# Optimization experiments

Measured on AMD Instinct MI355X. Metric: run time of the kernel, lower is better.

## Reference

```python
import jax, jax.numpy as jnp
import numpy as np

NUM_NODES = 512
HEADS = 4
IN_F = 256
OUT_F = 128
EPS = 1e-5


def _layernorm(x, g, b):
    mu = jnp.mean(x, axis=-1, keepdims=True)
    var = jnp.mean(jnp.square(x - mu), axis=-1, keepdims=True)
    return (x - mu) * jax.lax.rsqrt(var + EPS) * g + b


def setup_inputs() -> dict:
    key = jax.random.key(0)
    ks = jax.random.split(key, 16)
    N = 32 * NUM_NODES
    E = 262144
    s = 0.05
    return {
        "x": jax.random.normal(ks[0], (N, IN_F), jnp.float32),
        "edge_index": jax.random.randint(ks[1], (2, E), 0, N, jnp.int64),
        "W_l": jax.random.normal(ks[2], (IN_F, HEADS * OUT_F), jnp.float32) * s,
        "W_r": jax.random.normal(ks[3], (IN_F, HEADS * OUT_F), jnp.float32) * s,
        "att": jax.random.normal(ks[4], (HEADS, OUT_F), jnp.float32) * s,
        "gat_bias": jnp.zeros((OUT_F,), jnp.float32),
        "gat_gamma": jnp.ones((OUT_F,), jnp.float32),
        "gat_beta": jnp.zeros((OUT_F,), jnp.float32),
        "cnn_W": jax.random.normal(ks[5], (IN_F, OUT_F), jnp.float32) * s,
        "cnn_b": jnp.zeros((OUT_F,), jnp.float32),
        "conv_W": jax.random.normal(ks[6], (OUT_F, OUT_F, 7), jnp.float32) * s,
        "conv_b": jnp.zeros((OUT_F,), jnp.float32),
        "cnn_gamma": jnp.ones((OUT_F,), jnp.float32),
        "cnn_beta": jnp.zeros((OUT_F,), jnp.float32),
        "res_W": jax.random.normal(ks[7], (IN_F, OUT_F), jnp.float32) * s,
        "res_b": jnp.zeros((OUT_F,), jnp.float32),
        "fuse_gamma": jnp.ones((OUT_F,), jnp.float32),
        "fuse_beta": jnp.zeros((OUT_F,), jnp.float32),
    }


def reference(x, edge_index, W_l, W_r, att, gat_bias, gat_gamma, gat_beta,
              cnn_W, cnn_b, conv_W, conv_b, cnn_gamma, cnn_beta,
              res_W, res_b, fuse_gamma, fuse_beta):
    N = x.shape[0]
    B = N // NUM_NODES
    # --- GATv2 branch (add self-loops like PyG default) ---
    loop = jnp.arange(N, dtype=edge_index.dtype)
    src = jnp.concatenate([edge_index[0], loop])
    dst = jnp.concatenate([edge_index[1], loop])
    x_l = (x @ W_l).reshape(N, HEADS, OUT_F)
    x_r = (x @ W_r).reshape(N, HEADS, OUT_F)
    e = x_l[src] + x_r[dst]                      # [E+N, H, F]
    e = jnp.where(e > 0, e, 0.2 * e)             # leaky_relu, slope 0.2
    score = jnp.einsum('ehf,hf->eh', e, att)     # [E+N, H]
    m = jax.ops.segment_max(score, dst, num_segments=N)
    ex = jnp.exp(score - m[dst])
    denom = jax.ops.segment_sum(ex, dst, num_segments=N)
    alpha = ex / denom[dst]
    agg = jax.ops.segment_sum(alpha[:, :, None] * x_l[src], dst, num_segments=N)
    h_gat = jnp.mean(agg, axis=1) + gat_bias     # concat=False -> head mean
    h_gat = jnp.where(h_gat > 0, h_gat, 0.01 * h_gat)  # nn.LeakyReLU default
    h_gat = _layernorm(h_gat, gat_gamma, gat_beta)
    # --- CNN branch ---
    xc = x @ cnn_W + cnn_b                       # [N, F]
    xc = xc.reshape(B, NUM_NODES, OUT_F).transpose(0, 2, 1)  # [B, F, L]
    hc = jax.lax.conv_general_dilated(xc, conv_W, window_strides=(1,),
                                      padding=[(3, 3)],
                                      dimension_numbers=('NCW', 'OIW', 'NCW'))
    hc = hc + conv_b[None, :, None]
    hc = hc.transpose(0, 2, 1).reshape(N, OUT_F)
    hc = jax.nn.relu(hc)
    hc = _layernorm(hc, cnn_gamma, cnn_beta)
    # --- fuse + residual ---
    h = h_gat + hc + (x @ res_W + res_b)
    return _layernorm(h, fuse_gamma, fuse_beta)
```

## Files before the change

### kernel.cpp

```cpp
#include <hip/hip_runtime.h>
#include <hip/hip_bf16.h>
#include <math.h>

#define IN_F 256
#define OUT_F 128
#define HEADS 4
#define HF 512
#define NCAT 1280

typedef __hip_bfloat16 bf16;
typedef unsigned short ushort_t;
typedef unsigned char uchar_t;

using bf16x8 = __attribute__((ext_vector_type(8))) short;
using f32x4  = __attribute__((ext_vector_type(4))) float;

__device__ __forceinline__ float bflo(unsigned u) { return __uint_as_float(u << 16); }
__device__ __forceinline__ float bfhi(unsigned u) { return __uint_as_float(u & 0xffff0000u); }
__device__ __forceinline__ float bf2f(ushort_t u) { return __uint_as_float((unsigned)u << 16); }
__device__ __forceinline__ ushort_t f2bf(float f) {
    __hip_bfloat16 h = __float2bfloat16(f);
    return *reinterpret_cast<ushort_t*>(&h);
}

__device__ __forceinline__ void gload16(const void* g, void* l) {
    __builtin_amdgcn_global_load_lds(
        (const __attribute__((address_space(1))) unsigned int*)g,
        (__attribute__((address_space(3))) unsigned int*)l, 16, 0, 0);
}

template <int CTRL>
__device__ __forceinline__ float dpp_add(float s) {
    int t = __builtin_amdgcn_update_dpp(0, __float_as_int(s), CTRL, 0xf, 0xf, true);
    return s + __int_as_float(t);
}
__device__ __forceinline__ float rowsum16(float s) {
    s = dpp_add<0x121>(s);
    s = dpp_add<0x122>(s);
    s = dpp_add<0x124>(s);
    s = dpp_add<0x128>(s);
    return s;
}

__global__ __launch_bounds__(256) void prep_kernel(
    const float* __restrict__ x, ushort_t* __restrict__ xb, int n_cvt,
    const float* __restrict__ Wl, const float* __restrict__ Wr,
    const float* __restrict__ Wc, const float* __restrict__ Wres,
    const float* __restrict__ Wconv,
    ushort_t* __restrict__ Wt, ushort_t* __restrict__ Wt2,
    const int* __restrict__ ei, int* __restrict__ counts, int E,
    int g1, int g2) {
    int b = blockIdx.x;
    if (b < g1) {
        int i = (b * 256 + threadIdx.x) * 8;
        if (i >= n_cvt) return;
        float4 a = *(const float4*)(x + i);
        float4 c = *(const float4*)(x + i + 4);
        uint4 o;
        o.x = f2bf(a.x) | ((unsigned)f2bf(a.y) << 16);
        o.y = f2bf(a.z) | ((unsigned)f2bf(a.w) << 16);
        o.z = f2bf(c.x) | ((unsigned)f2bf(c.y) << 16);
        o.w = f2bf(c.z) | ((unsigned)f2bf(c.w) << 16);
        *(uint4*)(xb + i) = o;
    } else if (b < g2) {
        int idx = (b - g1) * 256 + threadIdx.x;
        if (idx < NCAT * 256) {
            int n = idx >> 8, k = idx & 255;
            float v;
            if (n < 512)       v = Wl[(size_t)k * 512 + n];
            else if (n < 1024) v = Wr[(size_t)k * 512 + (n - 512)];
            else if (n < 1152) v = Wc[(size_t)k * 128 + (n - 1024)];
            else               v = Wres[(size_t)k * 128 + (n - 1152)];
            Wt[idx] = f2bf(v);
        } else {
            int j = idx - NCAT * 256;
            if (j < 7 * 128 * 128) {
                int k = j >> 14, o = (j >> 7) & 127, i = j & 127;
                Wt2[j] = f2bf(Wconv[((size_t)o * 128 + i) * 7 + k]);
            }
        }
    } else {
        int e = (b - g2) * 256 + threadIdx.x;
        if (e < E) atomicAdd(&counts[ei[E + e]], 1);
    }
}

__global__ __launch_bounds__(256) void mfma_gemm(
    const ushort_t* __restrict__ A,
    const ushort_t* __restrict__ Wt,
    uchar_t* __restrict__ xl8t, float* __restrict__ scales,
    ushort_t* __restrict__ xrb, ushort_t* __restrict__ xcb,
    ushort_t* __restrict__ resb, int M) {
    __shared__ __align__(1024) ushort_t As[128 * 64];
    __shared__ __align__(1024) ushort_t Bs[128 * 64];
    __shared__ float smax[128][2];
    int tid = threadIdx.x;
    int lane = tid & 63, wid = tid >> 6;
    int wr = (wid >> 1) * 64, wc = (wid & 1) * 64;
    int brow = blockIdx.y * 128, bcol = blockIdx.x * 128;
    int srow = lane >> 3;
    int sslot = lane & 7;
    int rl = lane & 15, kq = lane >> 4;
    f32x4 acc[4][4] = {};
    for (int k0 = 0; k0 < 256; k0 += 64) {
        #pragma unroll
        for (int j = 0; j < 4; ++j) {
            int r = (wid * 4 + j) * 8 + srow;
            int sl = sslot ^ (r & 7);
            gload16(A  + (size_t)(brow + r) * 256 + k0 + sl * 8,
                    (char*)As + (wid * 4 + j) * 1024);
            gload16(Wt + (size_t)(bcol + r) * 256 + k0 + sl * 8,
                    (char*)Bs + (wid * 4 + j) * 1024);
        }
        __syncthreads();
        #pragma unroll
        for (int ks = 0; ks < 2; ++ks) {
            int cb = ks * 64 + kq * 16;
            bf16x8 af[4], bfv[4];
            #pragma unroll
            for (int m = 0; m < 4; ++m) {
                int r = wr + m * 16 + rl;
                af[m] = *(const bf16x8*)((const char*)As + r * 128 + (cb ^ ((r & 7) << 4)));
            }
            #pragma unroll
            for (int n = 0; n < 4; ++n) {
                int r = wc + n * 16 + rl;
                bfv[n] = *(const bf16x8*)((const char*)Bs + r * 128 + (cb ^ ((r & 7) << 4)));
            }
            #pragma unroll
            for (int m = 0; m < 4; ++m)
                #pragma unroll
                for (int n = 0; n < 4; ++n)
                    acc[m][n] = __builtin_amdgcn_mfma_f32_16x16x32_bf16(
                        af[m], bfv[n], acc[m][n], 0, 0, 0);
        }
        __syncthreads();
    }
    int rowb = kq * 4;
    if (bcol < 512) {
        int head = bcol >> 7;
        float rmax[4][4];
        #pragma unroll
        for (int m = 0; m < 4; ++m)
            #pragma unroll
            for (int q = 0; q < 4; ++q) {
                float t = fabsf(acc[m][0][q]);
                t = fmaxf(t, fabsf(acc[m][1][q]));
                t = fmaxf(t, fabsf(acc[m][2][q]));
                t = fmaxf(t, fabsf(acc[m][3][q]));
                #pragma unroll
                for (int o = 1; o < 16; o <<= 1) t = fmaxf(t, __shfl_xor(t, o));
                rmax[m][q] = t;
            }
        if (rl == 0) {
            #pragma unroll
            for (int m = 0; m < 4; ++m)
                #pragma unroll
                for (int q = 0; q < 4; ++q)
                    smax[wr + m * 16 + rowb + q][wid & 1] = rmax[m][q];
        }
        __syncthreads();
        #pragma unroll
        for (int m = 0; m < 4; ++m)
            #pragma unroll
            for (int q = 0; q < 4; ++q) {
                int row = wr + m * 16 + rowb + q;
                float sm = fmaxf(fmaxf(smax[row][0], smax[row][1]), 1e-8f);
                float s = sm * (1.f / 127.f);
                float rs = 127.f / sm;
                if ((wid & 1) == 0 && rl == 0)
                    scales[(size_t)(brow + row) * 4 + head] = s;
                #pragma unroll
                for (int n = 0; n < 4; ++n) {
                    int col = bcol + wc + n * 16 + rl;
                    int qv = (int)rintf(acc[m][n][q] * rs) + 128;
                    xl8t[(size_t)(brow + row) * 512 + col] = (uchar_t)qv;
                }
            }
        return;
    }
    ushort_t* dstp; int cstride, cb2;
    if (bcol < 1024)      { dstp = xrb;  cstride = 512; cb2 = bcol - 512; }
    else if (bcol < 1152) { dstp = xcb;  cstride = 128; cb2 = bcol - 1024; }
    else                  { dstp = resb; cstride = 128; cb2 = bcol - 1152; }
    #pragma unroll
    for (int m = 0; m < 4; ++m)
        #pragma unroll
        for (int n = 0; n < 4; ++n) {
            int col = cb2 + wc + n * 16 + rl;
            #pragma unroll
            for (int q = 0; q < 4; ++q) {
                int row = brow + wr + m * 16 + rowb + q;
                dstp[(size_t)row * cstride + col] = f2bf(acc[m][n][q]);
            }
        }
}

__global__ __launch_bounds__(1024) void scan_kernel(
    const int* __restrict__ counts, int* __restrict__ offs,
    int* __restrict__ cursor, int N) {
    __shared__ int wsum[16];
    int t = threadIdx.x;
    int lane = t & 63, w = t >> 6;
    int base = t * 16;
    int local[16], s = 0;
    #pragma unroll
    for (int i = 0; i < 16; ++i) {
        int v = (base + i < N) ? counts[base + i] : 0;
        local[i] = v; s += v;
    }
    int sc = s;
    #pragma unroll
    for (int off = 1; off < 64; off <<= 1) {
        int v = __shfl_up(sc, off);
        if (lane >= off) sc += v;
    }
    if (lane == 63) wsum[w] = sc;
    __syncthreads();
    if (w == 0 && lane < 16) {
        int v = wsum[lane];
        int scv = v;
        #pragma unroll
        for (int off = 1; off < 16; off <<= 1) {
            int u = __shfl_up(scv, off);
            if (lane >= off) scv += u;
        }
        wsum[lane] = scv - v;
    }
    __syncthreads();
    int run = wsum[w] + sc - s;
    #pragma unroll
    for (int i = 0; i < 16; ++i) {
        if (base + i < N) { offs[base + i] = run; cursor[base + i] = run; }
        run += local[i];
    }
}

__global__ __launch_bounds__(256) void scatter_kernel(
    const int* __restrict__ ei, int* __restrict__ cursor,
    int* __restrict__ srcs, int E) {
    int e = blockIdx.x * 256 + threadIdx.x;
    if (e < E) {
        int d = ei[E + e];
        int p = atomicAdd(&cursor[d], 1);
        srcs[p] = ei[e];
    }
}

__global__ __launch_bounds__(256) void conv_ln_kernel(
    const ushort_t* __restrict__ xcb, const float* __restrict__ cnn_b,
    const ushort_t* __restrict__ Wt2, const float* __restrict__ conv_b,
    const float* __restrict__ cnn_gamma, const float* __restrict__ cnn_beta,
    ushort_t* __restrict__ hcn_ln) {
    __shared__ ushort_t As[38][136];
    __shared__ __align__(1024) ushort_t Bs[128 * 128];
    __shared__ float hbuf[32][129];
    int tid = threadIdx.x;
    int lane = tid & 63, wid = tid >> 6;
    int wr = (wid >> 1) * 16, wc = (wid & 1) * 64;
    int b = blockIdx.y, l0 = blockIdx.x * 32;
    for (int u = tid; u < 38 * 16; u += 256) {
        int r = u >> 4, seg = u & 15;
        int l = l0 - 3 + r;
        uint4 o4 = make_uint4(0, 0, 0, 0);
        if (l >= 0 && l < 512) {
            uint4 v = *(const uint4*)(xcb + (size_t)(b * 512 + l) * 128 + seg * 8);
            float4 b0 = *(const float4*)(cnn_b + seg * 8);
            float4 b1 = *(const float4*)(cnn_b + seg * 8 + 4);
            o4.x = f2bf(bflo(v.x) + b0.x) | ((unsigned)f2bf(bfhi(v.x) + b0.y) << 16);
            o4.y = f2bf(bflo(v.y) + b0.z) | ((unsigned)f2bf(bfhi(v.y) + b0.w) << 16);
            o4.z = f2bf(bflo(v.z) + b1.x) | ((unsigned)f2bf(bfhi(v.z) + b1.y) << 16);
            o4.w = f2bf(bflo(v.w) + b1.z) | ((unsigned)f2bf(bfhi(v.w) + b1.w) << 16);
        }
        *(uint4*)&As[r][seg * 8] = o4;
    }
    f32x4 acc[4] = {};
    int rl = lane & 15, kb = (lane >> 4) * 8;
    int sr4 = lane >> 4, ss = lane & 15;
    for (int k = 0; k < 7; ++k) {
        __syncthreads();
        #pragma unroll
        for (int j = 0; j < 8; ++j) {
            int r = (wid * 8 + j) * 4 + sr4;
            int sl = ss ^ (r & 15);
            gload16(Wt2 + ((size_t)(k * 128 + r)) * 128 + sl * 8,
                    (char*)Bs + (wid * 8 + j) * 1024);
        }
        __syncthreads();
        #pragma unroll
        for (int kk = 0; kk < 4; ++kk) {
            bf16x8 af = *(const bf16x8*)&As[wr + rl + k][kk * 32 + kb];
            int cbyte = kk * 64 + (lane >> 4) * 16;
            #pragma unroll
            for (int n = 0; n < 4; ++n) {
                int r = wc + n * 16 + rl;
                bf16x8 bfr = *(const bf16x8*)((const char*)Bs + r * 256
                                              + (cbyte ^ ((r & 15) << 4)));
                acc[n] = __builtin_amdgcn_mfma_f32_16x16x32_bf16(af, bfr, acc[n], 0, 0, 0);
            }
        }
    }
    __syncthreads();
    int rowb = (lane >> 4) * 4;
    #pragma unroll
    for (int n = 0; n < 4; ++n) {
        int col = wc + n * 16 + rl;
        float cb = conv_b[col];
        #pragma unroll
        for (int q = 0; q < 4; ++q) {
            int r = wr + rowb + q;
            hbuf[r][col] = fmaxf(acc[n][q] + cb, 0.f);
        }
    }
    __syncthreads();
    for (int r = wid * 8; r < wid * 8 + 8; ++r) {
        int grow = b * 512 + l0 + r;
        float h0 = hbuf[r][lane], h1 = hbuf[r][lane + 64];
        float s = h0 + h1;
        #pragma unroll
        for (int off = 32; off; off >>= 1) s += __shfl_xor(s, off);
        float mu = s * (1.f / 128.f);
        float d0 = h0 - mu, d1 = h1 - mu;
        float vs = d0 * d0 + d1 * d1;
        #pragma unroll
        for (int off = 32; off; off >>= 1) vs += __shfl_xor(vs, off);
        float inv = rsqrtf(vs * (1.f / 128.f) + 1e-5f);
        size_t base = (size_t)grow * 128;
        hcn_ln[base + lane]      = f2bf(d0 * inv * cnn_gamma[lane]      + cnn_beta[lane]);
        hcn_ln[base + lane + 64] = f2bf(d1 * inv * cnn_gamma[lane + 64] + cnn_beta[lane + 64]);
    }
}

__global__ __launch_bounds__(256) void gat_final_kernel(
    const uchar_t* __restrict__ xl8t, const float* __restrict__ scales,
    const ushort_t* __restrict__ xrb,
    const int* __restrict__ srcs, const int* __restrict__ offs,
    const float* __restrict__ att, const float* __restrict__ gat_bias,
    const float* __restrict__ gat_gamma, const float* __restrict__ gat_beta,
    const ushort_t* __restrict__ hcn_ln, const ushort_t* __restrict__ resb,
    const float* __restrict__ res_b,
    const float* __restrict__ fuse_gamma, const float* __restrict__ fuse_beta,
    float* __restrict__ out, int E, int N) {
    int wid = (blockIdx.x * 256 + threadIdx.x) >> 6;
    int lane = threadIdx.x & 63;
    if (wid >= N) return;
    int d = wid;
    int h = lane >> 4;
    const uint4 rv = ((const uint4*)(xrb + (size_t)d * HF))[lane];
    float xr8[8];
    xr8[0] = bflo(rv.x); xr8[1] = bfhi(rv.x);
    xr8[2] = bflo(rv.y); xr8[3] = bfhi(rv.y);
    xr8[4] = bflo(rv.z); xr8[5] = bfhi(rv.z);
    xr8[6] = bflo(rv.w); xr8[7] = bfhi(rv.w);
    const float LOG2E = 1.44269504f;
    const float4 a0 = ((const float4*)att)[lane * 2];
    const float4 a1 = ((const float4*)att)[lane * 2 + 1];
    const float aw[8] = {a0.x * LOG2E, a0.y * LOG2E, a0.z * LOG2E, a0.w * LOG2E,
                         a1.x * LOG2E, a1.y * LOG2E, a1.z * LOG2E, a1.w * LOG2E};
    float acc[8] = {};
    float dn = 0.f, sumexs = 0.f;

    auto process = [&](uint2 lv, float sc) {
        float qf[8];
        qf[0] = (float)(lv.x & 0xff);         qf[1] = (float)((lv.x >> 8) & 0xff);
        qf[2] = (float)((lv.x >> 16) & 0xff); qf[3] = (float)(lv.x >> 24);
        qf[4] = (float)(lv.y & 0xff);         qf[5] = (float)((lv.y >> 8) & 0xff);
        qf[6] = (float)((lv.y >> 16) & 0xff); qf[7] = (float)(lv.y >> 24);
        float c = 128.f * sc;
        float s1 = 0.f, s2 = 0.f;
        #pragma unroll
        for (int j = 0; j < 8; ++j) {
            float v = fmaf(sc, qf[j], xr8[j]) - c;
            s1 = fmaf(v, aw[j], s1);
            s2 = fmaf(fabsf(v), aw[j], s2);
        }
        float s = fmaf(0.6f, s1, 0.4f * s2);
        s = rowsum16(s);
        float ex = exp2f(s);
        float exs = ex * sc;
        dn += ex; sumexs += exs;
        #pragma unroll
        for (int j = 0; j < 8; ++j) acc[j] = fmaf(exs, qf[j], acc[j]);
    };

    process(((const uint2*)(xl8t + (size_t)d * 512))[lane],
            scales[(size_t)d * 4 + h]);

    int start = offs[d];
    int end = (d == N - 1) ? E : offs[d + 1];
    int p = start;
    for (; p + 3 < end; p += 4) {
        int s0 = srcs[p], s1 = srcs[p + 1], s2 = srcs[p + 2], s3 = srcs[p + 3];
        uint2 l0 = ((const uint2*)(xl8t + (size_t)s0 * 512))[lane];
        uint2 l1 = ((const uint2*)(xl8t + (size_t)s1 * 512))[lane];
        uint2 l2 = ((const uint2*)(xl8t + (size_t)s2 * 512))[lane];
        uint2 l3 = ((const uint2*)(xl8t + (size_t)s3 * 512))[lane];
        float c0 = scales[(size_t)s0 * 4 + h];
        float c1 = scales[(size_t)s1 * 4 + h];
        float c2 = scales[(size_t)s2 * 4 + h];
        float c3 = scales[(size_t)s3 * 4 + h];
        process(l0, c0); process(l1, c1); process(l2, c2); process(l3, c3);
    }
    for (; p < end; ++p) {
        int sp = srcs[p];
        process(((const uint2*)(xl8t + (size_t)sp * 512))[lane],
                scales[(size_t)sp * 4 + h]);
    }

    float inv = 1.f / dn;
    float corr = 128.f * sumexs;
    float v[8];
    #pragma unroll
    for (int j = 0; j < 8; ++j) {
        float t2 = (acc[j] - corr) * inv;
        t2 += __shfl_xor(t2, 16);
        t2 += __shfl_xor(t2, 32);
        v[j] = t2;
    }
    int col = (lane & 15) * 8 + 2 * h;
    float g0 = 0.25f * v[2 * h]     + gat_bias[col];
    float g1 = 0.25f * v[2 * h + 1] + gat_bias[col + 1];
    g0 = g0 > 0.f ? g0 : 0.01f * g0;
    g1 = g1 > 0.f ? g1 : 0.01f * g1;
    float s = g0 + g1;
    #pragma unroll
    for (int off = 32; off; off >>= 1) s += __shfl_xor(s, off);
    float mu = s * (1.f / 128.f);
    float d0 = g0 - mu, d1 = g1 - mu;
    float vs = d0 * d0 + d1 * d1;
    #pragma unroll
    for (int off = 32; off; off >>= 1) vs += __shfl_xor(vs, off);
    float rinv = rsqrtf(vs * (1.f / 128.f) + 1e-5f);
    float hg0 = d0 * rinv * gat_gamma[col]     + gat_beta[col];
    float hg1 = d1 * rinv * gat_gamma[col + 1] + gat_beta[col + 1];
    size_t base = (size_t)d * 128 + col;
    unsigned hcu = *(const unsigned*)(hcn_ln + base);
    unsigned rsu = *(const unsigned*)(resb + base);
    float v0 = hg0 + bflo(hcu) + bflo(rsu) + res_b[col];
    float v1 = hg1 + bfhi(hcu) + bfhi(rsu) + res_b[col + 1];
    s = v0 + v1;
    #pragma unroll
    for (int off = 32; off; off >>= 1) s += __shfl_xor(s, off);
    mu = s * (1.f / 128.f);
    d0 = v0 - mu; d1 = v1 - mu;
    vs = d0 * d0 + d1 * d1;
    #pragma unroll
    for (int off = 32; off; off >>= 1) vs += __shfl_xor(vs, off);
    rinv = rsqrtf(vs * (1.f / 128.f) + 1e-5f);
    float2 o2 = make_float2(d0 * rinv * fuse_gamma[col]     + fuse_beta[col],
                            d1 * rinv * fuse_gamma[col + 1] + fuse_beta[col + 1]);
    *(float2*)(out + base) = o2;
}

extern "C" void kernel_launch(void* const* d_in, const int* in_sizes, int n_in,
                              void* d_out, int out_size, void* d_ws, size_t ws_size,
                              hipStream_t stream) {
    const float* x         = (const float*)d_in[0];
    const int*   ei        = (const int*)d_in[1];
    const float* W_l       = (const float*)d_in[2];
    const float* W_r       = (const float*)d_in[3];
    const float* att       = (const float*)d_in[4];
    const float* gat_bias  = (const float*)d_in[5];
    const float* gat_gamma = (const float*)d_in[6];
    const float* gat_beta  = (const float*)d_in[7];
    const float* cnn_W     = (const float*)d_in[8];
    const float* cnn_b     = (const float*)d_in[9];
    const float* conv_W    = (const float*)d_in[10];
    const float* conv_b    = (const float*)d_in[11];
    const float* cnn_gamma = (const float*)d_in[12];
    const float* cnn_beta  = (const float*)d_in[13];
    const float* res_W     = (const float*)d_in[14];
    const float* res_b     = (const float*)d_in[15];
    const float* fuse_gamma= (const float*)d_in[16];
    const float* fuse_beta = (const float*)d_in[17];

    int N = in_sizes[0] / IN_F;
    int E = in_sizes[1] / 2;

    char* ws = (char*)d_ws;
    size_t off = 0;
    ushort_t* xb     = (ushort_t*)(ws + off); off += (size_t)N * IN_F * 2;
    ushort_t* Wt     = (ushort_t*)(ws + off); off += (size_t)NCAT * IN_F * 2;
    ushort_t* Wt2    = (ushort_t*)(ws + off); off += (size_t)7 * 128 * 128 * 2;
    uchar_t*  xl8t   = (uchar_t*)(ws + off);  off += (size_t)N * HF;
    float*    scales = (float*)(ws + off);    off += (size_t)N * 4 * 4;
    ushort_t* xrb    = (ushort_t*)(ws + off); off += (size_t)N * HF * 2;
    ushort_t* xcb    = (ushort_t*)(ws + off); off += (size_t)N * 128 * 2;
    ushort_t* resb   = (ushort_t*)(ws + off); off += (size_t)N * 128 * 2;
    ushort_t* hcn_ln = (ushort_t*)(ws + off); off += (size_t)N * 128 * 2;
    int*  counts     = (int*)(ws + off);  off += (size_t)N * 4;
    int*  offs       = (int*)(ws + off);  off += (size_t)N * 4;
    int*  cursor     = (int*)(ws + off);  off += (size_t)N * 4;
    int*  srcs       = (int*)(ws + off);  off += (size_t)E * 4;

    hipMemsetAsync(counts, 0, (size_t)N * 4, stream);

    dim3 blk(256);
    int n_cvt = N * IN_F;
    int g1 = (n_cvt / 8 + 255) / 256;
    int g2 = g1 + (NCAT * 256 + 7 * 128 * 128 + 255) / 256;
    int g3 = g2 + (E + 255) / 256;
    prep_kernel<<<g3, blk, 0, stream>>>(x, xb, n_cvt,
        W_l, W_r, cnn_W, res_W, conv_W, Wt, Wt2, ei, counts, E, g1, g2);

    scan_kernel<<<1, 1024, 0, stream>>>(counts, offs, cursor, N);
    scatter_kernel<<<(E + 255) / 256, blk, 0, stream>>>(ei, cursor, srcs, E);

    mfma_gemm<<<dim3(NCAT / 128, N / 128), blk, 0, stream>>>(
        xb, Wt, xl8t, scales, xrb, xcb, resb, N);

    conv_ln_kernel<<<dim3(16, 32), blk, 0, stream>>>(
        xcb, cnn_b, Wt2, conv_b, cnn_gamma, cnn_beta, hcn_ln);

    gat_final_kernel<<<(N + 3) / 4, blk, 0, stream>>>(
        xl8t, scales, xrb, srcs, offs, att, gat_bias, gat_gamma, gat_beta,
        hcn_ln, resb, res_b, fuse_gamma, fuse_beta, (float*)d_out, E, N);
}
```

Before: 142.3 us.

## Split each node's edge list across two waves and combine via shared memory

```diff
diff --git a/kernel.cpp b/kernel.cpp
--- a/kernel.cpp
+++ b/kernel.cpp
@@ -341,10 +341,11 @@
     const float* __restrict__ res_b,
     const float* __restrict__ fuse_gamma, const float* __restrict__ fuse_beta,
     float* __restrict__ out, int E, int N) {
-    int wid = (blockIdx.x * 256 + threadIdx.x) >> 6;
-    int lane = threadIdx.x & 63;
-    if (wid >= N) return;
-    int d = wid;
+    __shared__ float comb[2][10][64];
+    int tid = threadIdx.x;
+    int lane = tid & 63, wid = tid >> 6;
+    int pair = wid >> 1, half = wid & 1;
+    int d = blockIdx.x * 2 + pair;
     int h = lane >> 4;
     const uint4 rv = ((const uint4*)(xrb + (size_t)d * HF))[lane];
     float xr8[8];
@@ -383,13 +384,17 @@
         for (int j = 0; j < 8; ++j) acc[j] = fmaf(exs, qf[j], acc[j]);
     };
 
-    process(((const uint2*)(xl8t + (size_t)d * 512))[lane],
-            scales[(size_t)d * 4 + h]);
+    if (half == 0)
+        process(((const uint2*)(xl8t + (size_t)d * 512))[lane],
+                scales[(size_t)d * 4 + h]);
 
     int start = offs[d];
     int end = (d == N - 1) ? E : offs[d + 1];
-    int p = start;
-    for (; p + 3 < end; p += 4) {
+    int mid = start + ((end - start) >> 1);
+    int ps = half ? mid : start;
+    int pe = half ? end : mid;
+    int p = ps;
+    for (; p + 3 < pe; p += 4) {
         int s0 = srcs[p], s1 = srcs[p + 1], s2 = srcs[p + 2], s3 = srcs[p + 3];
         uint2 l0 = ((const uint2*)(xl8t + (size_t)s0 * 512))[lane];
         uint2 l1 = ((const uint2*)(xl8t + (size_t)s1 * 512))[lane];
@@ -401,11 +406,24 @@
         float c3 = scales[(size_t)s3 * 4 + h];
         process(l0, c0); process(l1, c1); process(l2, c2); process(l3, c3);
     }
-    for (; p < end; ++p) {
+    for (; p < pe; ++p) {
         int sp = srcs[p];
         process(((const uint2*)(xl8t + (size_t)sp * 512))[lane],
                 scales[(size_t)sp * 4 + h]);
     }
+
+    if (half == 1) {
+        #pragma unroll
+        for (int j = 0; j < 8; ++j) comb[pair][j][lane] = acc[j];
+        comb[pair][8][lane] = dn;
+        comb[pair][9][lane] = sumexs;
+    }
+    __syncthreads();
+    if (half == 1) return;
+    #pragma unroll
+    for (int j = 0; j < 8; ++j) acc[j] += comb[pair][j][lane];
+    dn += comb[pair][8][lane];
+    sumexs += comb[pair][9][lane];
 
     float inv = 1.f / dn;
     float corr = 128.f * sumexs;
@@ -512,7 +530,7 @@
     conv_ln_kernel<<<dim3(16, 32), blk, 0, stream>>>(
         xcb, cnn_b, Wt2, conv_b, cnn_gamma, cnn_beta, hcn_ln);
 
-    gat_final_kernel<<<(N + 3) / 4, blk, 0, stream>>>(
+    gat_final_kernel<<<N / 2, blk, 0, stream>>>(
         xl8t, scales, xrb, srcs, offs, att, gat_bias, gat_gamma, gat_beta,
         hcn_ln, resb, res_b, fuse_gamma, fuse_beta, (float*)d_out, E, N);
 }
```

Result: slower. 153.5 us (+7.9%).

## Merge edge scatter into GEMM launch and software-pipeline GAT neighbor loads

Applied to the files above, without the earlier changes.

```diff
diff --git a/kernel.cpp b/kernel.cpp
--- a/kernel.cpp
+++ b/kernel.cpp
@@ -85,19 +85,32 @@
     }
 }
 
-__global__ __launch_bounds__(256) void mfma_gemm(
+__global__ __launch_bounds__(256) void gemm_scatter_kernel(
     const ushort_t* __restrict__ A,
     const ushort_t* __restrict__ Wt,
     uchar_t* __restrict__ xl8t, float* __restrict__ scales,
     ushort_t* __restrict__ xrb, ushort_t* __restrict__ xcb,
-    ushort_t* __restrict__ resb, int M) {
+    ushort_t* __restrict__ resb,
+    const int* __restrict__ ei, int* __restrict__ cursor,
+    int* __restrict__ srcs, int E, int SB) {
     __shared__ __align__(1024) ushort_t As[128 * 64];
     __shared__ __align__(1024) ushort_t Bs[128 * 64];
     __shared__ float smax[128][2];
+    if (blockIdx.x < SB) {
+        int e = blockIdx.x * 256 + threadIdx.x;
+        if (e < E) {
+            int dd = ei[E + e];
+            int pp = atomicAdd(&cursor[dd], 1);
+            srcs[pp] = ei[e];
+        }
+        return;
+    }
+    int bid = blockIdx.x - SB;
+    int by = bid / 10, bx = bid - by * 10;
     int tid = threadIdx.x;
     int lane = tid & 63, wid = tid >> 6;
     int wr = (wid >> 1) * 64, wc = (wid & 1) * 64;
-    int brow = blockIdx.y * 128, bcol = blockIdx.x * 128;
+    int brow = by * 128, bcol = bx * 128;
     int srow = lane >> 3;
     int sslot = lane & 7;
     int rl = lane & 15, kq = lane >> 4;
@@ -233,17 +246,6 @@
     for (int i = 0; i < 16; ++i) {
         if (base + i < N) { offs[base + i] = run; cursor[base + i] = run; }
         run += local[i];
-    }
-}
-
-__global__ __launch_bounds__(256) void scatter_kernel(
-    const int* __restrict__ ei, int* __restrict__ cursor,
-    int* __restrict__ srcs, int E) {
-    int e = blockIdx.x * 256 + threadIdx.x;
-    if (e < E) {
-        int d = ei[E + e];
-        int p = atomicAdd(&cursor[d], 1);
-        srcs[p] = ei[e];
     }
 }
 
@@ -388,18 +390,39 @@
 
     int start = offs[d];
     int end = (d == N - 1) ? E : offs[d + 1];
+    int nfull = (end - start) >> 2;
     int p = start;
-    for (; p + 3 < end; p += 4) {
+    uint2 L0, L1, L2, L3;
+    float C0, C1, C2, C3;
+    if (nfull > 0) {
         int s0 = srcs[p], s1 = srcs[p + 1], s2 = srcs[p + 2], s3 = srcs[p + 3];
-        uint2 l0 = ((const uint2*)(xl8t + (size_t)s0 * 512))[lane];
-        uint2 l1 = ((const uint2*)(xl8t + (size_t)s1 * 512))[lane];
-        uint2 l2 = ((const uint2*)(xl8t + (size_t)s2 * 512))[lane];
-        uint2 l3 = ((const uint2*)(xl8t + (size_t)s3 * 512))[lane];
-        float c0 = scales[(size_t)s0 * 4 + h];
-        float c1 = scales[(size_t)s1 * 4 + h];
-        float c2 = scales[(size_t)s2 * 4 + h];
-        float c3 = scales[(size_t)s3 * 4 + h];
-        process(l0, c0); process(l1, c1); process(l2, c2); process(l3, c3);
+        L0 = ((const uint2*)(xl8t + (size_t)s0 * 512))[lane];
+        L1 = ((const uint2*)(xl8t + (size_t)s1 * 512))[lane];
+        L2 = ((const uint2*)(xl8t + (size_t)s2 * 512))[lane];
+        L3 = ((const uint2*)(xl8t + (size_t)s3 * 512))[lane];
+        C0 = scales[(size_t)s0 * 4 + h];
+        C1 = scales[(size_t)s1 * 4 + h];
+        C2 = scales[(size_t)s2 * 4 + h];
+        C3 = scales[(size_t)s3 * 4 + h];
+        p += 4;
+    }
+    for (int b = 1; b < nfull; ++b) {
+        int s0 = srcs[p], s1 = srcs[p + 1], s2 = srcs[p + 2], s3 = srcs[p + 3];
+        uint2 M0 = ((const uint2*)(xl8t + (size_t)s0 * 512))[lane];
+        uint2 M1 = ((const uint2*)(xl8t + (size_t)s1 * 512))[lane];
+        uint2 M2 = ((const uint2*)(xl8t + (size_t)s2 * 512))[lane];
+        uint2 M3 = ((const uint2*)(xl8t + (size_t)s3 * 512))[lane];
+        float D0 = scales[(size_t)s0 * 4 + h];
+        float D1 = scales[(size_t)s1 * 4 + h];
+        float D2 = scales[(size_t)s2 * 4 + h];
+        float D3 = scales[(size_t)s3 * 4 + h];
+        p += 4;
+        process(L0, C0); process(L1, C1); process(L2, C2); process(L3, C3);
+        L0 = M0; L1 = M1; L2 = M2; L3 = M3;
+        C0 = D0; C1 = D1; C2 = D2; C3 = D3;
+    }
+    if (nfull > 0) {
+        process(L0, C0); process(L1, C1); process(L2, C2); process(L3, C3);
     }
     for (; p < end; ++p) {
         int sp = srcs[p];
@@ -504,10 +527,10 @@
         W_l, W_r, cnn_W, res_W, conv_W, Wt, Wt2, ei, counts, E, g1, g2);
 
     scan_kernel<<<1, 1024, 0, stream>>>(counts, offs, cursor, N);
-    scatter_kernel<<<(E + 255) / 256, blk, 0, stream>>>(ei, cursor, srcs, E);
-
-    mfma_gemm<<<dim3(NCAT / 128, N / 128), blk, 0, stream>>>(
-        xb, Wt, xl8t, scales, xrb, xcb, resb, N);
+
+    int SB = (E + 255) / 256;
+    gemm_scatter_kernel<<<SB + (NCAT / 128) * (N / 128), blk, 0, stream>>>(
+        xb, Wt, xl8t, scales, xrb, xcb, resb, ei, cursor, srcs, E, SB);
 
     conv_ln_kernel<<<dim3(16, 32), blk, 0, stream>>>(
         xcb, cnn_b, Wt2, conv_b, cnn_gamma, cnn_beta, hcn_ln);
```

After: 139.5 us. -2.0%, faster.

## Merge independent kernels into heterogeneous launches and split out final fuse layernorm

Applied to the files above, without the earlier changes.

```diff
diff --git a/kernel.cpp b/kernel.cpp
--- a/kernel.cpp
+++ b/kernel.cpp
@@ -85,19 +85,32 @@
     }
 }
 
-__global__ __launch_bounds__(256) void mfma_gemm(
+__global__ __launch_bounds__(256) void gemm_scatter_kernel(
     const ushort_t* __restrict__ A,
     const ushort_t* __restrict__ Wt,
     uchar_t* __restrict__ xl8t, float* __restrict__ scales,
     ushort_t* __restrict__ xrb, ushort_t* __restrict__ xcb,
-    ushort_t* __restrict__ resb, int M) {
+    ushort_t* __restrict__ resb,
+    const int* __restrict__ ei, int* __restrict__ cursor,
+    int* __restrict__ srcs, int E, int SB) {
     __shared__ __align__(1024) ushort_t As[128 * 64];
     __shared__ __align__(1024) ushort_t Bs[128 * 64];
     __shared__ float smax[128][2];
+    if (blockIdx.x < SB) {
+        int e = blockIdx.x * 256 + threadIdx.x;
+        if (e < E) {
+            int dd = ei[E + e];
+            int pp = atomicAdd(&cursor[dd], 1);
+            srcs[pp] = ei[e];
+        }
+        return;
+    }
+    int bid = blockIdx.x - SB;
+    int by = bid / 10, bx = bid - by * 10;
     int tid = threadIdx.x;
     int lane = tid & 63, wid = tid >> 6;
     int wr = (wid >> 1) * 64, wc = (wid & 1) * 64;
-    int brow = blockIdx.y * 128, bcol = blockIdx.x * 128;
+    int brow = by * 128, bcol = bx * 128;
     int srow = lane >> 3;
     int sslot = lane & 7;
     int rl = lane & 15, kq = lane >> 4;
@@ -236,115 +249,103 @@
     }
 }
 
-__global__ __launch_bounds__(256) void scatter_kernel(
-    const int* __restrict__ ei, int* __restrict__ cursor,
-    int* __restrict__ srcs, int E) {
-    int e = blockIdx.x * 256 + threadIdx.x;
-    if (e < E) {
-        int d = ei[E + e];
-        int p = atomicAdd(&cursor[d], 1);
-        srcs[p] = ei[e];
-    }
-}
-
-__global__ __launch_bounds__(256) void conv_ln_kernel(
+#define CONV_BLOCKS 512
+__global__ __launch_bounds__(256) void conv_gat_kernel(
     const ushort_t* __restrict__ xcb, const float* __restrict__ cnn_b,
     const ushort_t* __restrict__ Wt2, const float* __restrict__ conv_b,
     const float* __restrict__ cnn_gamma, const float* __restrict__ cnn_beta,
-    ushort_t* __restrict__ hcn_ln) {
-    __shared__ ushort_t As[38][136];
-    __shared__ __align__(1024) ushort_t Bs[128 * 128];
-    __shared__ float hbuf[32][129];
-    int tid = threadIdx.x;
-    int lane = tid & 63, wid = tid >> 6;
-    int wr = (wid >> 1) * 16, wc = (wid & 1) * 64;
-    int b = blockIdx.y, l0 = blockIdx.x * 32;
-    for (int u = tid; u < 38 * 16; u += 256) {
-        int r = u >> 4, seg = u & 15;
-        int l = l0 - 3 + r;
-        uint4 o4 = make_uint4(0, 0, 0, 0);
-        if (l >= 0 && l < 512) {
-            uint4 v = *(const uint4*)(xcb + (size_t)(b * 512 + l) * 128 + seg * 8);
-            float4 b0 = *(const float4*)(cnn_b + seg * 8);
-            float4 b1 = *(const float4*)(cnn_b + seg * 8 + 4);
-            o4.x = f2bf(bflo(v.x) + b0.x) | ((unsigned)f2bf(bfhi(v.x) + b0.y) << 16);
-            o4.y = f2bf(bflo(v.y) + b0.z) | ((unsigned)f2bf(bfhi(v.y) + b0.w) << 16);
-            o4.z = f2bf(bflo(v.z) + b1.x) | ((unsigned)f2bf(bfhi(v.z) + b1.y) << 16);
-            o4.w = f2bf(bflo(v.w) + b1.z) | ((unsigned)f2bf(bfhi(v.w) + b1.w) << 16);
-        }
-        *(uint4*)&As[r][seg * 8] = o4;
-    }
-    f32x4 acc[4] = {};
-    int rl = lane & 15, kb = (lane >> 4) * 8;
-    int sr4 = lane >> 4, ss = lane & 15;
-    for (int k = 0; k < 7; ++k) {
-        __syncthreads();
-        #pragma unroll
-        for (int j = 0; j < 8; ++j) {
-            int r = (wid * 8 + j) * 4 + sr4;
-            int sl = ss ^ (r & 15);
-            gload16(Wt2 + ((size_t)(k * 128 + r)) * 128 + sl * 8,
-                    (char*)Bs + (wid * 8 + j) * 1024);
-        }
-        __syncthreads();
-        #pragma unroll
-        for (int kk = 0; kk < 4; ++kk) {
-            bf16x8 af = *(const bf16x8*)&As[wr + rl + k][kk * 32 + kb];
-            int cbyte = kk * 64 + (lane >> 4) * 16;
-            #pragma unroll
-            for (int n = 0; n < 4; ++n) {
-                int r = wc + n * 16 + rl;
-                bf16x8 bfr = *(const bf16x8*)((const char*)Bs + r * 256
-                                              + (cbyte ^ ((r & 15) << 4)));
-                acc[n] = __builtin_amdgcn_mfma_f32_16x16x32_bf16(af, bfr, acc[n], 0, 0, 0);
-            }
-        }
-    }
-    __syncthreads();
-    int rowb = (lane >> 4) * 4;
-    #pragma unroll
-    for (int n = 0; n < 4; ++n) {
-        int col = wc + n * 16 + rl;
-        float cb = conv_b[col];
-        #pragma unroll
-        for (int q = 0; q < 4; ++q) {
-            int r = wr + rowb + q;
-            hbuf[r][col] = fmaxf(acc[n][q] + cb, 0.f);
-        }
-    }
-    __syncthreads();
-    for (int r = wid * 8; r < wid * 8 + 8; ++r) {
-        int grow = b * 512 + l0 + r;
-        float h0 = hbuf[r][lane], h1 = hbuf[r][lane + 64];
-        float s = h0 + h1;
-        #pragma unroll
-        for (int off = 32; off; off >>= 1) s += __shfl_xor(s, off);
-        float mu = s * (1.f / 128.f);
-        float d0 = h0 - mu, d1 = h1 - mu;
-        float vs = d0 * d0 + d1 * d1;
-        #pragma unroll
-        for (int off = 32; off; off >>= 1) vs += __shfl_xor(vs, off);
-        float inv = rsqrtf(vs * (1.f / 128.f) + 1e-5f);
-        size_t base = (size_t)grow * 128;
-        hcn_ln[base + lane]      = f2bf(d0 * inv * cnn_gamma[lane]      + cnn_beta[lane]);
-        hcn_ln[base + lane + 64] = f2bf(d1 * inv * cnn_gamma[lane + 64] + cnn_beta[lane + 64]);
-    }
-}
-
-__global__ __launch_bounds__(256) void gat_final_kernel(
+    ushort_t* __restrict__ hcn_ln,
     const uchar_t* __restrict__ xl8t, const float* __restrict__ scales,
     const ushort_t* __restrict__ xrb,
     const int* __restrict__ srcs, const int* __restrict__ offs,
     const float* __restrict__ att, const float* __restrict__ gat_bias,
     const float* __restrict__ gat_gamma, const float* __restrict__ gat_beta,
-    const ushort_t* __restrict__ hcn_ln, const ushort_t* __restrict__ resb,
-    const float* __restrict__ res_b,
-    const float* __restrict__ fuse_gamma, const float* __restrict__ fuse_beta,
-    float* __restrict__ out, int E, int N) {
-    int wid = (blockIdx.x * 256 + threadIdx.x) >> 6;
-    int lane = threadIdx.x & 63;
-    if (wid >= N) return;
-    int d = wid;
+    ushort_t* __restrict__ hgat_ln, int E, int N) {
+    __shared__ __align__(1024) char smem[43104];
+    int tid = threadIdx.x;
+    int lane = tid & 63, wid = tid >> 6;
+
+    if (blockIdx.x < CONV_BLOCKS) {
+        ushort_t* Bs = (ushort_t*)smem;
+        ushort_t (*As)[136] = (ushort_t(*)[136])(smem + 32768);
+        int wr = (wid >> 1) * 16, wc = (wid & 1) * 64;
+        int b = blockIdx.x >> 4, l0 = (blockIdx.x & 15) * 32;
+        for (int u = tid; u < 38 * 16; u += 256) {
+            int r = u >> 4, seg = u & 15;
+            int l = l0 - 3 + r;
+            uint4 o4 = make_uint4(0, 0, 0, 0);
+            if (l >= 0 && l < 512) {
+                uint4 v = *(const uint4*)(xcb + (size_t)(b * 512 + l) * 128 + seg * 8);
+                float4 b0 = *(const float4*)(cnn_b + seg * 8);
+                float4 b1 = *(const float4*)(cnn_b + seg * 8 + 4);
+                o4.x = f2bf(bflo(v.x) + b0.x) | ((unsigned)f2bf(bfhi(v.x) + b0.y) << 16);
+                o4.y = f2bf(bflo(v.y) + b0.z) | ((unsigned)f2bf(bfhi(v.y) + b0.w) << 16);
+                o4.z = f2bf(bflo(v.z) + b1.x) | ((unsigned)f2bf(bfhi(v.z) + b1.y) << 16);
+                o4.w = f2bf(bflo(v.w) + b1.z) | ((unsigned)f2bf(bfhi(v.w) + b1.w) << 16);
+            }
+            *(uint4*)&As[r][seg * 8] = o4;
+        }
+        f32x4 acc[4] = {};
+        int rl = lane & 15, kb = (lane >> 4) * 8;
+        int sr4 = lane >> 4, ss = lane & 15;
+        for (int k = 0; k < 7; ++k) {
+            __syncthreads();
+            #pragma unroll
+            for (int j = 0; j < 8; ++j) {
+                int r = (wid * 8 + j) * 4 + sr4;
+                int sl = ss ^ (r & 15);
+                gload16(Wt2 + ((size_t)(k * 128 + r)) * 128 + sl * 8,
+                        (char*)Bs + (wid * 8 + j) * 1024);
+            }
+            __syncthreads();
+            #pragma unroll
+            for (int kk = 0; kk < 4; ++kk) {
+                bf16x8 af = *(const bf16x8*)&As[wr + rl + k][kk * 32 + kb];
+                int cbyte = kk * 64 + (lane >> 4) * 16;
+                #pragma unroll
+                for (int n = 0; n < 4; ++n) {
+                    int r = wc + n * 16 + rl;
+                    bf16x8 bfr = *(const bf16x8*)((const char*)Bs + r * 256
+                                                  + (cbyte ^ ((r & 15) << 4)));
+                    acc[n] = __builtin_amdgcn_mfma_f32_16x16x32_bf16(af, bfr, acc[n], 0, 0, 0);
+                }
+            }
+        }
+        __syncthreads();
+        float (*hbuf)[129] = (float(*)[129])smem;
+        int rowb = (lane >> 4) * 4;
+        #pragma unroll
+        for (int n = 0; n < 4; ++n) {
+            int col = wc + n * 16 + rl;
+            float cb = conv_b[col];
+            #pragma unroll
+            for (int q = 0; q < 4; ++q) {
+                int r = wr + rowb + q;
+                hbuf[r][col] = fmaxf(acc[n][q] + cb, 0.f);
+            }
+        }
+        __syncthreads();
+        for (int r = wid * 8; r < wid * 8 + 8; ++r) {
+            int grow = b * 512 + l0 + r;
+            float h0 = hbuf[r][lane], h1 = hbuf[r][lane + 64];
+            float s = h0 + h1;
+            #pragma unroll
+            for (int off = 32; off; off >>= 1) s += __shfl_xor(s, off);
+            float mu = s * (1.f / 128.f);
+            float d0 = h0 - mu, d1 = h1 - mu;
+            float vs = d0 * d0 + d1 * d1;
+            #pragma unroll
+            for (int off = 32; off; off >>= 1) vs += __shfl_xor(vs, off);
+            float inv = rsqrtf(vs * (1.f / 128.f) + 1e-5f);
+            size_t base = (size_t)grow * 128;
+            hcn_ln[base + lane]      = f2bf(d0 * inv * cnn_gamma[lane]      + cnn_beta[lane]);
+            hcn_ln[base + lane + 64] = f2bf(d1 * inv * cnn_gamma[lane + 64] + cnn_beta[lane + 64]);
+        }
+        return;
+    }
+
+    int d = (blockIdx.x - CONV_BLOCKS) * 4 + wid;
+    if (d >= N) return;
     int h = lane >> 4;
     const uint4 rv = ((const uint4*)(xrb + (size_t)d * HF))[lane];
     float xr8[8];
@@ -431,25 +432,36 @@
     #pragma unroll
     for (int off = 32; off; off >>= 1) vs += __shfl_xor(vs, off);
     float rinv = rsqrtf(vs * (1.f / 128.f) + 1e-5f);
-    float hg0 = d0 * rinv * gat_gamma[col]     + gat_beta[col];
-    float hg1 = d1 * rinv * gat_gamma[col + 1] + gat_beta[col + 1];
-    size_t base = (size_t)d * 128 + col;
-    unsigned hcu = *(const unsigned*)(hcn_ln + base);
-    unsigned rsu = *(const unsigned*)(resb + base);
-    float v0 = hg0 + bflo(hcu) + bflo(rsu) + res_b[col];
-    float v1 = hg1 + bfhi(hcu) + bfhi(rsu) + res_b[col + 1];
-    s = v0 + v1;
+    float o0 = d0 * rinv * gat_gamma[col]     + gat_beta[col];
+    float o1 = d1 * rinv * gat_gamma[col + 1] + gat_beta[col + 1];
+    unsigned pk = (unsigned)f2bf(o0) | ((unsigned)f2bf(o1) << 16);
+    *(unsigned*)(hgat_ln + (size_t)d * 128 + col) = pk;
+}
+
+__global__ __launch_bounds__(256) void fuse_ln_kernel(
+    const ushort_t* __restrict__ hgat_ln, const ushort_t* __restrict__ hcn_ln,
+    const ushort_t* __restrict__ resb, const float* __restrict__ res_b,
+    const float* __restrict__ fuse_gamma, const float* __restrict__ fuse_beta,
+    float* __restrict__ out, int N) {
+    int wid = (blockIdx.x * 256 + threadIdx.x) >> 6;
+    int lane = threadIdx.x & 63;
+    if (wid >= N) return;
+    size_t base = (size_t)wid * 128;
+    float v0 = bf2f(hgat_ln[base + lane])      + bf2f(hcn_ln[base + lane])
+             + bf2f(resb[base + lane])         + res_b[lane];
+    float v1 = bf2f(hgat_ln[base + lane + 64]) + bf2f(hcn_ln[base + lane + 64])
+             + bf2f(resb[base + lane + 64])    + res_b[lane + 64];
+    float s = v0 + v1;
     #pragma unroll
     for (int off = 32; off; off >>= 1) s += __shfl_xor(s, off);
-    mu = s * (1.f / 128.f);
-    d0 = v0 - mu; d1 = v1 - mu;
-    vs = d0 * d0 + d1 * d1;
+    float mu = s * (1.f / 128.f);
+    float d0 = v0 - mu, d1 = v1 - mu;
+    float vs = d0 * d0 + d1 * d1;
     #pragma unroll
     for (int off = 32; off; off >>= 1) vs += __shfl_xor(vs, off);
-    rinv = rsqrtf(vs * (1.f / 128.f) + 1e-5f);
-    float2 o2 = make_float2(d0 * rinv * fuse_gamma[col]     + fuse_beta[col],
-                            d1 * rinv * fuse_gamma[col + 1] + fuse_beta[col + 1]);
-    *(float2*)(out + base) = o2;
+    float inv = rsqrtf(vs * (1.f / 128.f) + 1e-5f);
+    out[base + lane]      = d0 * inv * fuse_gamma[lane]      + fuse_beta[lane];
+    out[base + lane + 64] = d1 * inv * fuse_gamma[lane + 64] + fuse_beta[lane + 64];
 }
 
 extern "C" void kernel_launch(void* const* d_in, const int* in_sizes, int n_in,
@@ -488,6 +500,7 @@
     ushort_t* xcb    = (ushort_t*)(ws + off); off += (size_t)N * 128 * 2;
     ushort_t* resb   = (ushort_t*)(ws + off); off += (size_t)N * 128 * 2;
     ushort_t* hcn_ln = (ushort_t*)(ws + off); off += (size_t)N * 128 * 2;
+    ushort_t* hgat_ln= (ushort_t*)(ws + off); off += (size_t)N * 128 * 2;
     int*  counts     = (int*)(ws + off);  off += (size_t)N * 4;
     int*  offs       = (int*)(ws + off);  off += (size_t)N * 4;
     int*  cursor     = (int*)(ws + off);  off += (size_t)N * 4;
@@ -504,15 +517,16 @@
         W_l, W_r, cnn_W, res_W, conv_W, Wt, Wt2, ei, counts, E, g1, g2);
 
     scan_kernel<<<1, 1024, 0, stream>>>(counts, offs, cursor, N);
-    scatter_kernel<<<(E + 255) / 256, blk, 0, stream>>>(ei, cursor, srcs, E);
-
-    mfma_gemm<<<dim3(NCAT / 128, N / 128), blk, 0, stream>>>(
-        xb, Wt, xl8t, scales, xrb, xcb, resb, N);
-
-    conv_ln_kernel<<<dim3(16, 32), blk, 0, stream>>>(
-        xcb, cnn_b, Wt2, conv_b, cnn_gamma, cnn_beta, hcn_ln);
-
-    gat_final_kernel<<<(N + 3) / 4, blk, 0, stream>>>(
+
+    int SB = (E + 255) / 256;
+    gemm_scatter_kernel<<<SB + (NCAT / 128) * (N / 128), blk, 0, stream>>>(
+        xb, Wt, xl8t, scales, xrb, xcb, resb, ei, cursor, srcs, E, SB);
+
+    conv_gat_kernel<<<CONV_BLOCKS + (N + 3) / 4, blk, 0, stream>>>(
+        xcb, cnn_b, Wt2, conv_b, cnn_gamma, cnn_beta, hcn_ln,
         xl8t, scales, xrb, srcs, offs, att, gat_bias, gat_gamma, gat_beta,
-        hcn_ln, resb, res_b, fuse_gamma, fuse_beta, (float*)d_out, E, N);
-}
+        hgat_ln, E, N);
+
+    fuse_ln_kernel<<<(N + 3) / 4, blk, 0, stream>>>(
+        hgat_ln, hcn_ln, resb, res_b, fuse_gamma, fuse_beta, (float*)d_out, N);
+}
```

New measurement: 147.8 us. 3.9% more time.
